# Optimization experiments

Measured on AMD Instinct MI355X. Metric: run time of the kernel, lower is better.

## Reference

```python
import jax, jax.numpy as jnp
import numpy as np

CLIP_LIMIT = 40.0
TILES = 8  # tileGridSize=(8,8)
BINS = 256


def masked_normalize(x, mask, lo, hi):
    # Faithful to Preprocessor.normalize: if mask nonempty and masked max>0,
    # rescale masked values from [vmin,vmax] -> [lo,hi]; else set masked to lo.
    vmax = jnp.max(jnp.where(mask, x, -jnp.inf))
    vmin = jnp.min(jnp.where(mask, x, jnp.inf))
    cond = jnp.any(mask) & (vmax > 0.0)
    rng = jnp.maximum(vmax - vmin, jnp.float32(1e-12))  # guard degenerate case
    scaled = (x - vmin) / rng * (hi - lo) + lo
    return jnp.where(mask, jnp.where(cond, scaled, jnp.float32(lo)), x)


def clahe_apply(img, clip_limit, T):
    # img: (H, W) int32 in [0, 255]. OpenCV-style CLAHE: per-tile clipped
    # histogram equalization LUTs + bilinear interpolation between tile LUTs.
    H, W = img.shape
    th, tw = H // T, W // T
    area = th * tw
    # per-tile histograms via segment_sum (memory-light, no one-hot blowup)
    ty = jnp.arange(H, dtype=jnp.int32) // th
    tx = jnp.arange(W, dtype=jnp.int32) // tw
    tile_id = ty[:, None] * T + tx[None, :]  # (H, W)
    seg = (tile_id * BINS + img).reshape(-1)
    hist = jax.ops.segment_sum(
        jnp.ones(H * W, jnp.float32), seg, num_segments=T * T * BINS
    ).reshape(T * T, BINS)
    # clip + redistribute excess (uniform batch + stepped residual, OpenCV-style)
    cl = max(int(clip_limit * area / BINS), 1)
    excess = jnp.sum(jnp.maximum(hist - cl, 0.0), axis=1, keepdims=True)
    hist = jnp.minimum(hist, float(cl))
    batch = jnp.floor(excess / BINS)
    residual = excess - batch * BINS  # in [0, 256)
    ar = jnp.arange(BINS, dtype=jnp.float32)
    step = jnp.maximum(jnp.floor(BINS / jnp.maximum(residual, 1.0)), 1.0)
    res_add = ((jnp.mod(ar, step) == 0.0) & (jnp.floor(ar / step) < residual)).astype(jnp.float32)
    hist = hist + batch + res_add
    # LUT from CDF
    cdf = jnp.cumsum(hist, axis=1)
    lut = jnp.clip(jnp.round(cdf * (255.0 / area)), 0.0, 255.0).reshape(T, T, BINS)
    # bilinear interpolation between the 4 surrounding tile LUTs
    fy = (jnp.arange(H, dtype=jnp.float32) + 0.5) / th - 0.5
    fx = (jnp.arange(W, dtype=jnp.float32) + 0.5) / tw - 0.5
    y0 = jnp.clip(jnp.floor(fy).astype(jnp.int32), 0, T - 1)
    x0 = jnp.clip(jnp.floor(fx).astype(jnp.int32), 0, T - 1)
    y1 = jnp.clip(y0 + 1, 0, T - 1)
    x1 = jnp.clip(x0 + 1, 0, T - 1)
    wy = (fy - jnp.floor(fy))[:, None]  # (H,1); at clamped borders both LUTs equal
    wx = (fx - jnp.floor(fx))[None, :]  # (1,W)
    v00 = lut[y0[:, None], x0[None, :], img]
    v01 = lut[y0[:, None], x1[None, :], img]
    v10 = lut[y1[:, None], x0[None, :], img]
    v11 = lut[y1[:, None], x1[None, :], img]
    return (v00 * (1 - wy) * (1 - wx) + v01 * (1 - wy) * wx
            + v10 * wy * (1 - wx) + v11 * wy * wx)


def contrast(x):
    # (X*255).to(uint8) truncates; values in [0,1] so plain floor + clip
    xb = jnp.clip(jnp.floor(x * 255.0), 0.0, 255.0).astype(jnp.int32)
    zero = xb == 0
    nz_cnt = jnp.sum(~zero)
    mean_nz = jnp.floor(
        jnp.sum(jnp.where(zero, 0, xb).astype(jnp.float32)) / jnp.maximum(nz_cnt, 1)
    ).astype(jnp.int32)
    filled = jnp.where(zero & (nz_cnt > 0), mean_nz, xb)
    eq = clahe_apply(filled, CLIP_LIMIT, TILES)
    eq = jnp.where(zero, 0.0, eq)
    return eq / 255.0


def _process_channel(x):  # x: (H, W)
    mask = x > 0.0
    x = masked_normalize(x, mask, 0.0, 1.0)
    x = contrast(x)
    x = masked_normalize(x, mask, 1.0 / 255.0, 1.0)
    return x


def setup_inputs() -> dict:
    key = jax.random.key(0)
    X = jax.random.uniform(key, (1, 4, 4096, 4096), dtype=jnp.float32)
    return {"X": X}


def reference(X):
    # X: (1, C, H, W); channels are processed independently
    out = jax.vmap(_process_channel)(X[0])
    return out[None]
```

## Files before the change

kernel.cpp:

```cpp
#include <hip/hip_runtime.h>
#include <stdint.h>
#include <math.h>

#define NPC 16777216
#define NF4 4194304

typedef float f32x4 __attribute__((ext_vector_type(4)));

struct ChScalars {
  int vmin1, vmax1;
  int vmin2, vmax2;
  int mean_nz, nzpos;
  int pad0, pad1;
};

__device__ __forceinline__ int binof(float x, int cond1, float vmin, float rng) {
  float t = (x > 0.0f) ? (cond1 ? (x - vmin) / rng : 0.0f) : x;
  float b = floorf(t * 255.0f);
  b = fminf(fmaxf(b, 0.0f), 255.0f);
  return (int)b;
}

__global__ __launch_bounds__(256) void k_init(ChScalars* S, unsigned* hist) {
  int g = blockIdx.x * 256 + threadIdx.x;
  hist[g] = 0u;
  if (g < 4) {
    S[g].vmin1 = 0x7FFFFFFF;
    S[g].vmax1 = 0;
    S[g].vmin2 = 0x7FFFFFFF;
    S[g].vmax2 = 0x80000000;
    S[g].mean_nz = 0;
    S[g].nzpos = 0;
    S[g].pad0 = 0; S[g].pad1 = 0;
  }
}

__global__ __launch_bounds__(256) void k_minmax1(const float* __restrict__ X,
                                                 ChScalars* __restrict__ S) {
  const int ch = blockIdx.y;
  const float4* xp = reinterpret_cast<const float4*>(X) + (size_t)ch * NF4;
  const int g = blockIdx.x * 256 + threadIdx.x;
  int mn = 0x7FFFFFFF, mx = 0;
  #pragma unroll
  for (int i = 0; i < 16; ++i) {
    float4 v = xp[(size_t)i * 262144 + g];
    if (v.x > 0.0f) { int b = __float_as_int(v.x); mn = min(mn, b); mx = max(mx, b); }
    if (v.y > 0.0f) { int b = __float_as_int(v.y); mn = min(mn, b); mx = max(mx, b); }
    if (v.z > 0.0f) { int b = __float_as_int(v.z); mn = min(mn, b); mx = max(mx, b); }
    if (v.w > 0.0f) { int b = __float_as_int(v.w); mn = min(mn, b); mx = max(mx, b); }
  }
  __shared__ int smn[256], smx[256];
  smn[threadIdx.x] = mn; smx[threadIdx.x] = mx;
  __syncthreads();
  for (int st = 128; st > 0; st >>= 1) {
    if (threadIdx.x < st) {
      smn[threadIdx.x] = min(smn[threadIdx.x], smn[threadIdx.x + st]);
      smx[threadIdx.x] = max(smx[threadIdx.x], smx[threadIdx.x + st]);
    }
    __syncthreads();
  }
  if (threadIdx.x == 0) {
    atomicMin(&S[ch].vmin1, smn[0]);
    atomicMax(&S[ch].vmax1, smx[0]);
  }
}

__global__ __launch_bounds__(256) void k_hist(const float* __restrict__ X,
                                              const ChScalars* __restrict__ S,
                                              unsigned* __restrict__ hist) {
  const int ch = blockIdx.z;
  __shared__ unsigned lh[256];
  lh[threadIdx.x] = 0u;
  __syncthreads();
  const ChScalars s = S[ch];
  const int cond1 = s.vmax1 > 0;
  const float vmin = __int_as_float(s.vmin1);
  const float rng = fmaxf(__int_as_float(s.vmax1) - vmin, 1e-12f);
  const int X0 = (15 - (int)blockIdx.x) << 8;
  const int Y0 = (63 - (int)blockIdx.y) << 6;
  const float4* xp = reinterpret_cast<const float4*>(X) + (size_t)ch * NF4;
  for (int i = 0; i < 16; ++i) {
    int fidx = i * 256 + threadIdx.x;
    int r = fidx >> 6, c4 = fidx & 63;
    float4 v = xp[(size_t)(Y0 + r) * 1024 + (X0 >> 2) + c4];
    atomicAdd(&lh[binof(v.x, cond1, vmin, rng)], 1u);
    atomicAdd(&lh[binof(v.y, cond1, vmin, rng)], 1u);
    atomicAdd(&lh[binof(v.z, cond1, vmin, rng)], 1u);
    atomicAdd(&lh[binof(v.w, cond1, vmin, rng)], 1u);
  }
  __syncthreads();
  const int tile = ((Y0 >> 9) << 3) + (X0 >> 9);
  atomicAdd(&hist[((ch << 6) + tile) * 256 + threadIdx.x], lh[threadIdx.x]);
}

__global__ __launch_bounds__(256) void k_lut(const unsigned* __restrict__ hist,
                                             ChScalars* __restrict__ S,
                                             float* __restrict__ lut) {
  const int ch = blockIdx.y, tile = blockIdx.x, b = threadIdx.x;
  unsigned long long cnt = 0;
  for (int t = 0; t < 64; ++t) cnt += hist[((ch << 6) + t) * 256 + b];
  __shared__ unsigned long long sh64[256];
  __shared__ unsigned zc;
  if (b == 0) zc = (unsigned)cnt;
  sh64[b] = (b == 0) ? 0ULL : (unsigned long long)b * cnt;
  __syncthreads();
  for (int st = 128; st > 0; st >>= 1) {
    if (b < st) sh64[b] += sh64[b + st];
    __syncthreads();
  }
  const long long nz = 16777216LL - (long long)zc;
  const float sumf = (float)sh64[0];
  const long long d = (nz < 1) ? 1 : nz;
  const int mean_nz = (int)floor((double)sumf / (double)d);
  const int nzpos = (nz > 0) ? 1 : 0;
  if (tile == 0 && b == 0) { S[ch].mean_nz = mean_nz; S[ch].nzpos = nzpos; }
  const unsigned* hrow = hist + ((ch << 6) + tile) * 256;
  float h = (float)hrow[b];
  if (nzpos && mean_nz != 0) {
    unsigned h0 = hrow[0];
    if (b == 0) h = 0.0f;
    if (b == mean_nz) h += (float)h0;
  }
  __shared__ float sh[256];
  sh[b] = fmaxf(h - 40960.0f, 0.0f);
  __syncthreads();
  for (int st = 128; st > 0; st >>= 1) {
    if (b < st) sh[b] += sh[b + st];
    __syncthreads();
  }
  const float excess = sh[0];
  __syncthreads();
  float hc = fminf(h, 40960.0f);
  float batch = floorf(excess / 256.0f);
  float residual = excess - batch * 256.0f;
  float step = fmaxf(floorf(256.0f / fmaxf(residual, 1.0f)), 1.0f);
  float fb = (float)b;
  float res_add = ((fmodf(fb, step) == 0.0f) && (floorf(fb / step) < residual)) ? 1.0f : 0.0f;
  sh[b] = hc + batch + res_add;
  __syncthreads();
  for (int st = 1; st < 256; st <<= 1) {
    float v = (b >= st) ? sh[b - st] : 0.0f;
    __syncthreads();
    sh[b] += v;
    __syncthreads();
  }
  float l = rintf(sh[b] * (255.0f / 262144.0f));
  lut[((ch << 6) + tile) * 256 + b] = fminf(fmaxf(l, 0.0f), 255.0f);
}

template <bool WRITE>
__global__ __launch_bounds__(256) void k_apply(const float* __restrict__ X,
                                               const ChScalars* __restrict__ Sin,
                                               const float* __restrict__ lut,
                                               ChScalars* __restrict__ Smut,
                                               float* __restrict__ out) {
  const int ch = blockIdx.z;
  const int bx = WRITE ? (15 - (int)blockIdx.x) : (int)blockIdx.x;
  const int by = WRITE ? (63 - (int)blockIdx.y) : (int)blockIdx.y;
  const int X0 = bx << 8, Y0 = by << 6;
  const ChScalars s = Sin[ch];
  const int cond1 = s.vmax1 > 0;
  const float vmin = __int_as_float(s.vmin1);
  const float rng = fmaxf(__int_as_float(s.vmax1) - vmin, 1e-12f);
  const int iy0 = (Y0 < 256) ? -1 : ((Y0 - 256) >> 9);
  const int ix0 = (X0 < 256) ? -1 : ((X0 - 256) >> 9);
  const int y0t = (iy0 < 0) ? 0 : iy0;
  const int y1t = (iy0 + 1 > 7) ? 7 : (iy0 + 1);
  const int x0t = (ix0 < 0) ? 0 : ix0;
  const int x1t = (ix0 + 1 > 7) ? 7 : (ix0 + 1);
  __shared__ f32x4 L4[256];
  {
    const float* lc = lut + (size_t)(ch << 6) * 256;
    f32x4 Lv;
    Lv.x = lc[(y0t * 8 + x0t) * 256 + threadIdx.x];
    Lv.y = lc[(y0t * 8 + x1t) * 256 + threadIdx.x];
    Lv.z = lc[(y1t * 8 + x0t) * 256 + threadIdx.x];
    Lv.w = lc[(y1t * 8 + x1t) * 256 + threadIdx.x];
    L4[threadIdx.x] = Lv;
  }
  __syncthreads();
  const float vmax2c = __int_as_float(s.vmax2) / 255.0f;
  const float vmin2c = __int_as_float(s.vmin2) / 255.0f;
  const int cond2 = (s.vmax1 > 0) && (vmax2c > 0.0f);
  const float rng2 = fmaxf(vmax2c - vmin2c, 1e-12f);
  const float LO = (float)(1.0 / 255.0);
  const float SC = (float)(1.0 - 1.0 / 255.0);
  const int c4 = threadIdx.x & 63;
  const int r0 = threadIdx.x >> 6;
  float wxk[4], omwxk[4];
  #pragma unroll
  for (int k = 0; k < 4; ++k) {
    float fx = ((float)(X0 + (c4 << 2) + k) + 0.5f) / 512.0f - 0.5f;
    float w = fx - floorf(fx);
    wxk[k] = w;
    omwxk[k] = 1.0f - w;
  }
  const float4* xp = reinterpret_cast<const float4*>(X) + (size_t)ch * NF4;
  float* op = WRITE ? (out + (size_t)ch * NPC) : nullptr;
  int mn = 0x7FFFFFFF, mx = 0x80000000;
  for (int i = 0; i < 16; ++i) {
    const int y = Y0 + i * 4 + r0;
    const size_t f4i = (size_t)y * 1024 + (X0 >> 2) + c4;
    const float4 v = xp[f4i];
    const float fy = ((float)y + 0.5f) / 512.0f - 0.5f;
    const float wy = fy - floorf(fy);
    const float omwy = 1.0f - wy;
    float vv[4] = {v.x, v.y, v.z, v.w};
    float res[4];
    #pragma unroll
    for (int k = 0; k < 4; ++k) {
      float xv = vv[k];
      int xb = binof(xv, cond1, vmin, rng);
      int zero = (xb == 0);
      int f = (zero && s.nzpos) ? s.mean_nz : xb;
      f32x4 Lv = L4[f];
      float eq = Lv.x * omwy * omwxk[k]
               + Lv.y * omwy * wxk[k]
               + Lv.z * wy * omwxk[k]
               + Lv.w * wy * wxk[k];
      if (zero) eq = 0.0f;
      if (WRITE) {
        float cval = eq / 255.0f;
        float o;
        if (xv > 0.0f) o = cond2 ? ((cval - vmin2c) / rng2 * SC + LO) : LO;
        else o = cval;
        res[k] = o;
      } else {
        if (xv > 0.0f) {
          int bb = __float_as_int(eq);
          mn = min(mn, bb);
          mx = max(mx, bb);
        }
      }
    }
    if (WRITE) {
      f32x4 o4 = {res[0], res[1], res[2], res[3]};
      __builtin_nontemporal_store(o4, reinterpret_cast<f32x4*>(op) + f4i);
    }
  }
  if (!WRITE) {
    __shared__ int smn[256], smx[256];
    smn[threadIdx.x] = mn; smx[threadIdx.x] = mx;
    __syncthreads();
    for (int st = 128; st > 0; st >>= 1) {
      if (threadIdx.x < st) {
        smn[threadIdx.x] = min(smn[threadIdx.x], smn[threadIdx.x + st]);
        smx[threadIdx.x] = max(smx[threadIdx.x], smx[threadIdx.x + st]);
      }
      __syncthreads();
    }
    if (threadIdx.x == 0) {
      atomicMin(&Smut[ch].vmin2, smn[0]);
      atomicMax(&Smut[ch].vmax2, smx[0]);
    }
  }
}

extern "C" void kernel_launch(void* const* d_in, const int* in_sizes, int n_in,
                              void* d_out, int out_size, void* d_ws, size_t ws_size,
                              hipStream_t stream) {
  const float* X = (const float*)d_in[0];
  float* out = (float*)d_out;
  char* ws = (char*)d_ws;
  ChScalars* S = (ChScalars*)ws;
  unsigned* hist = (unsigned*)(ws + 256);
  float* lut = (float*)(ws + 256 + 65536 * 4);

  k_init<<<256, 256, 0, stream>>>(S, hist);
  k_minmax1<<<dim3(1024, 4, 1), 256, 0, stream>>>(X, S);
  k_hist<<<dim3(16, 64, 4), 256, 0, stream>>>(X, S, hist);
  k_lut<<<dim3(64, 4, 1), 256, 0, stream>>>(hist, S, lut);
  k_apply<false><<<dim3(16, 64, 4), 256, 0, stream>>>(X, S, lut, S, nullptr);
  k_apply<true><<<dim3(16, 64, 4), 256, 0, stream>>>(X, S, lut, S, out);
}
```

Before: 668.5 us.

## Cache packed bin indices as u16 in histogram pass for apply passes

The histogram kernel now writes a compact 16-bit code per pixel: the bin plus a positivity flag. Both apply passes read these codes instead of re-reading the float input and recomputing the bin, which halves their input traffic. The local histogram is also split into four per-wave copies to reduce shared atomic contention. In exchange, the histogram pass gains an extra write of half the input size and needs more workspace.

```diff
diff --git a/kernel.cpp b/kernel.cpp
--- a/kernel.cpp
+++ b/kernel.cpp
@@ -4,8 +4,11 @@
 
 #define NPC 16777216
 #define NF4 4194304
+#define NF8 2097152
 
 typedef float f32x4 __attribute__((ext_vector_type(4)));
+typedef unsigned short u16x4 __attribute__((ext_vector_type(4)));
+typedef unsigned short u16x8 __attribute__((ext_vector_type(8)));
 
 struct ChScalars {
   int vmin1, vmax1;
@@ -67,10 +70,13 @@
 
 __global__ __launch_bounds__(256) void k_hist(const float* __restrict__ X,
                                               const ChScalars* __restrict__ S,
-                                              unsigned* __restrict__ hist) {
+                                              unsigned* __restrict__ hist,
+                                              unsigned short* __restrict__ B) {
   const int ch = blockIdx.z;
-  __shared__ unsigned lh[256];
-  lh[threadIdx.x] = 0u;
+  __shared__ unsigned lh[4][256];
+  const int w = threadIdx.x >> 6;
+  #pragma unroll
+  for (int q = 0; q < 4; ++q) lh[q][threadIdx.x] = 0u;
   __syncthreads();
   const ChScalars s = S[ch];
   const int cond1 = s.vmax1 > 0;
@@ -79,18 +85,32 @@
   const int X0 = (15 - (int)blockIdx.x) << 8;
   const int Y0 = (63 - (int)blockIdx.y) << 6;
   const float4* xp = reinterpret_cast<const float4*>(X) + (size_t)ch * NF4;
+  u16x4* Bp4 = reinterpret_cast<u16x4*>(B) + (size_t)ch * NF4;
   for (int i = 0; i < 16; ++i) {
     int fidx = i * 256 + threadIdx.x;
     int r = fidx >> 6, c4 = fidx & 63;
-    float4 v = xp[(size_t)(Y0 + r) * 1024 + (X0 >> 2) + c4];
-    atomicAdd(&lh[binof(v.x, cond1, vmin, rng)], 1u);
-    atomicAdd(&lh[binof(v.y, cond1, vmin, rng)], 1u);
-    atomicAdd(&lh[binof(v.z, cond1, vmin, rng)], 1u);
-    atomicAdd(&lh[binof(v.w, cond1, vmin, rng)], 1u);
+    size_t f4i = (size_t)(Y0 + r) * 1024 + (X0 >> 2) + c4;
+    float4 v = xp[f4i];
+    int b0 = binof(v.x, cond1, vmin, rng);
+    int b1 = binof(v.y, cond1, vmin, rng);
+    int b2 = binof(v.z, cond1, vmin, rng);
+    int b3 = binof(v.w, cond1, vmin, rng);
+    u16x4 bv;
+    bv.x = (unsigned short)(b0 | ((v.x > 0.0f) ? 256 : 0));
+    bv.y = (unsigned short)(b1 | ((v.y > 0.0f) ? 256 : 0));
+    bv.z = (unsigned short)(b2 | ((v.z > 0.0f) ? 256 : 0));
+    bv.w = (unsigned short)(b3 | ((v.w > 0.0f) ? 256 : 0));
+    Bp4[f4i] = bv;
+    atomicAdd(&lh[w][b0], 1u);
+    atomicAdd(&lh[w][b1], 1u);
+    atomicAdd(&lh[w][b2], 1u);
+    atomicAdd(&lh[w][b3], 1u);
   }
   __syncthreads();
   const int tile = ((Y0 >> 9) << 3) + (X0 >> 9);
-  atomicAdd(&hist[((ch << 6) + tile) * 256 + threadIdx.x], lh[threadIdx.x]);
+  unsigned tot = lh[0][threadIdx.x] + lh[1][threadIdx.x]
+               + lh[2][threadIdx.x] + lh[3][threadIdx.x];
+  atomicAdd(&hist[((ch << 6) + tile) * 256 + threadIdx.x], tot);
 }
 
 __global__ __launch_bounds__(256) void k_lut(const unsigned* __restrict__ hist,
@@ -149,7 +169,7 @@
 }
 
 template <bool WRITE>
-__global__ __launch_bounds__(256) void k_apply(const float* __restrict__ X,
+__global__ __launch_bounds__(256) void k_apply(const unsigned short* __restrict__ B,
                                                const ChScalars* __restrict__ Sin,
                                                const float* __restrict__ lut,
                                                ChScalars* __restrict__ Smut,
@@ -159,9 +179,6 @@
   const int by = WRITE ? (63 - (int)blockIdx.y) : (int)blockIdx.y;
   const int X0 = bx << 8, Y0 = by << 6;
   const ChScalars s = Sin[ch];
-  const int cond1 = s.vmax1 > 0;
-  const float vmin = __int_as_float(s.vmin1);
-  const float rng = fmaxf(__int_as_float(s.vmax1) - vmin, 1e-12f);
   const int iy0 = (Y0 < 256) ? -1 : ((Y0 - 256) >> 9);
   const int ix0 = (X0 < 256) ? -1 : ((X0 - 256) >> 9);
   const int y0t = (iy0 < 0) ? 0 : iy0;
@@ -185,34 +202,33 @@
   const float rng2 = fmaxf(vmax2c - vmin2c, 1e-12f);
   const float LO = (float)(1.0 / 255.0);
   const float SC = (float)(1.0 - 1.0 / 255.0);
-  const int c4 = threadIdx.x & 63;
-  const int r0 = threadIdx.x >> 6;
-  float wxk[4], omwxk[4];
+  const int c8 = threadIdx.x & 31;
+  const int r0 = threadIdx.x >> 5;
+  float wxk[8], omwxk[8];
   #pragma unroll
-  for (int k = 0; k < 4; ++k) {
-    float fx = ((float)(X0 + (c4 << 2) + k) + 0.5f) / 512.0f - 0.5f;
-    float w = fx - floorf(fx);
-    wxk[k] = w;
-    omwxk[k] = 1.0f - w;
-  }
-  const float4* xp = reinterpret_cast<const float4*>(X) + (size_t)ch * NF4;
+  for (int k = 0; k < 8; ++k) {
+    float fx = ((float)(X0 + (c8 << 3) + k) + 0.5f) / 512.0f - 0.5f;
+    float ww = fx - floorf(fx);
+    wxk[k] = ww;
+    omwxk[k] = 1.0f - ww;
+  }
+  const u16x8* Bp = reinterpret_cast<const u16x8*>(B) + (size_t)ch * NF8;
   float* op = WRITE ? (out + (size_t)ch * NPC) : nullptr;
   int mn = 0x7FFFFFFF, mx = 0x80000000;
-  for (int i = 0; i < 16; ++i) {
-    const int y = Y0 + i * 4 + r0;
-    const size_t f4i = (size_t)y * 1024 + (X0 >> 2) + c4;
-    const float4 v = xp[f4i];
+  for (int i = 0; i < 8; ++i) {
+    const int y = Y0 + i * 8 + r0;
+    const u16x8 bv = Bp[(size_t)y * 512 + (X0 >> 3) + c8];
     const float fy = ((float)y + 0.5f) / 512.0f - 0.5f;
     const float wy = fy - floorf(fy);
     const float omwy = 1.0f - wy;
-    float vv[4] = {v.x, v.y, v.z, v.w};
-    float res[4];
+    float res[8];
     #pragma unroll
-    for (int k = 0; k < 4; ++k) {
-      float xv = vv[k];
-      int xb = binof(xv, cond1, vmin, rng);
-      int zero = (xb == 0);
-      int f = (zero && s.nzpos) ? s.mean_nz : xb;
+    for (int k = 0; k < 8; ++k) {
+      const int bm = bv[k];
+      const int xb = bm & 255;
+      const int msk = bm >> 8;
+      const int zero = (xb == 0);
+      const int f = (zero && s.nzpos) ? s.mean_nz : xb;
       f32x4 Lv = L4[f];
       float eq = Lv.x * omwy * omwxk[k]
                + Lv.y * omwy * wxk[k]
@@ -221,12 +237,9 @@
       if (zero) eq = 0.0f;
       if (WRITE) {
         float cval = eq / 255.0f;
-        float o;
-        if (xv > 0.0f) o = cond2 ? ((cval - vmin2c) / rng2 * SC + LO) : LO;
-        else o = cval;
-        res[k] = o;
+        res[k] = msk ? (cond2 ? ((cval - vmin2c) / rng2 * SC + LO) : LO) : cval;
       } else {
-        if (xv > 0.0f) {
+        if (msk) {
           int bb = __float_as_int(eq);
           mn = min(mn, bb);
           mx = max(mx, bb);
@@ -234,8 +247,11 @@
       }
     }
     if (WRITE) {
-      f32x4 o4 = {res[0], res[1], res[2], res[3]};
-      __builtin_nontemporal_store(o4, reinterpret_cast<f32x4*>(op) + f4i);
+      f32x4 o0 = {res[0], res[1], res[2], res[3]};
+      f32x4 o1 = {res[4], res[5], res[6], res[7]};
+      size_t o4i = (size_t)y * 1024 + (X0 >> 2) + (c8 << 1);
+      __builtin_nontemporal_store(o0, reinterpret_cast<f32x4*>(op) + o4i);
+      __builtin_nontemporal_store(o1, reinterpret_cast<f32x4*>(op) + o4i + 1);
     }
   }
   if (!WRITE) {
@@ -265,11 +281,12 @@
   ChScalars* S = (ChScalars*)ws;
   unsigned* hist = (unsigned*)(ws + 256);
   float* lut = (float*)(ws + 256 + 65536 * 4);
+  unsigned short* B = (unsigned short*)(ws + 256 + 65536 * 8);
 
   k_init<<<256, 256, 0, stream>>>(S, hist);
   k_minmax1<<<dim3(1024, 4, 1), 256, 0, stream>>>(X, S);
-  k_hist<<<dim3(16, 64, 4), 256, 0, stream>>>(X, S, hist);
+  k_hist<<<dim3(16, 64, 4), 256, 0, stream>>>(X, S, hist, B);
   k_lut<<<dim3(64, 4, 1), 256, 0, stream>>>(hist, S, lut);
-  k_apply<false><<<dim3(16, 64, 4), 256, 0, stream>>>(X, S, lut, S, nullptr);
-  k_apply<true><<<dim3(16, 64, 4), 256, 0, stream>>>(X, S, lut, S, out);
-}
+  k_apply<false><<<dim3(16, 64, 4), 256, 0, stream>>>(B, S, lut, S, nullptr);
+  k_apply<true><<<dim3(16, 64, 4), 256, 0, stream>>>(B, S, lut, S, out);
+}
```

Result: slower. 695.5 us (+4.0%).
